# Optimization experiments

Hardware: AMD Instinct MI355X
Metric: run time of the kernel (lower is better)

The kernel has to match this reference:

```python
import jax, jax.numpy as jnp
import numpy as np

B, T, D, H = 4, 1024, 1024, 16
TP = 1024
HD = D // H
LN_EPS = 1e-3  # keras LayerNormalization default epsilon


def snac_linear(x, wt, mt):
    # conv1dsnac: w = tanh(wt) * sigmoid(mt), shape [1, nx, nf] -> [nx, nf]
    w = (jnp.tanh(wt) * jax.nn.sigmoid(mt))[0]
    return jnp.einsum('btx,xf->btf', x, w)


def layernorm(x, gamma, beta):
    mu = jnp.mean(x, axis=-1, keepdims=True)
    var = jnp.mean(jnp.square(x - mu), axis=-1, keepdims=True)
    return (x - mu) * jax.lax.rsqrt(var + LN_EPS) * gamma + beta


def setup_inputs() -> dict:
    key = jax.random.key(0)
    ks = jax.random.split(key, 10)
    s = 0.02
    return {
        'input': jax.random.normal(ks[0], (B, T, D), jnp.float32),
        'past': jax.random.normal(ks[1], (B, 2, H, TP, HD), jnp.float32),
        'qkv_wt': jax.random.normal(ks[2], (1, D, 3 * D), jnp.float32) * s,
        'qkv_mt': jax.random.normal(ks[3], (1, D, 3 * D), jnp.float32) * s,
        'merge_wt': jax.random.normal(ks[4], (1, D, D), jnp.float32) * s,
        'merge_mt': jax.random.normal(ks[5], (1, D, D), jnp.float32) * s,
        'ln1_wt': jax.random.normal(ks[6], (1, D, D), jnp.float32) * s,
        'ln1_mt': jax.random.normal(ks[7], (1, D, D), jnp.float32) * s,
        'g1': jnp.ones((D,), jnp.float32), 'b1': jnp.zeros((D,), jnp.float32),
        'g2': jnp.ones((D,), jnp.float32), 'b2': jnp.zeros((D,), jnp.float32),
    }


def reference(input, past, qkv_wt, qkv_mt, merge_wt, merge_mt, ln1_wt, ln1_mt, g1, b1, g2, b2):
    x = input
    xn = layernorm(x, g1, b1)
    c = snac_linear(xn, qkv_wt, qkv_mt)  # [B, T, 3D]
    q, k, v = jnp.split(c, 3, axis=2)
    # split heads -> [B, H, T, HD]
    to_heads = lambda t: t.reshape(B, T, H, HD).transpose(0, 2, 1, 3)
    q, k, v = to_heads(q), to_heads(k), to_heads(v)
    present = jnp.stack([k, v], axis=1)  # [B, 2, H, T, HD]
    pk, pv = past[:, 0], past[:, 1]
    k = jnp.concatenate([pk, k], axis=2)  # [B, H, TP+T, HD]
    v = jnp.concatenate([pv, v], axis=2)
    nd, ns = T, TP + T
    w = jnp.einsum('bhqd,bhkd->bhqk', q, k) * jax.lax.rsqrt(jnp.float32(HD))
    i = jnp.arange(nd)[:, None]
    j = jnp.arange(ns)[None, :]
    m = (i >= j - ns + nd).astype(w.dtype)  # [nd, ns] causal mask incl. past
    w = w * m - jnp.asarray(1e10, w.dtype) * (1 - m)
    msk = jax.nn.softmax(w, axis=-1)  # [B, H, T, TP+T]
    a = jnp.einsum('bhqk,bhkd->bhqd', msk, v)
    ah = a.transpose(0, 2, 1, 3).reshape(B, T, D)  # merge heads
    am = snac_linear(ah, merge_wt, merge_mt)
    xa = x + am
    mlp = snac_linear(layernorm(xa, g2, b2), ln1_wt, ln1_mt)
    xm = xa + mlp
    return xm, present, msk
```

## Files before the change

### kernel.cpp

```cpp
#include <hip/hip_runtime.h>
#include <hip/hip_bf16.h>

typedef _Float16 half8 __attribute__((ext_vector_type(8)));
typedef _Float16 half4v __attribute__((ext_vector_type(4)));
typedef float f32x4 __attribute__((ext_vector_type(4)));

#define DEV static __device__ __forceinline__


typedef __attribute__((address_space(1))) const unsigned int* gas_p;
typedef __attribute__((address_space(3))) unsigned int* las_p;
DEV void glds16(const void* g, void* s) {
  __builtin_amdgcn_global_load_lds((gas_p)g, (las_p)s, 16, 0, 0);
}

__global__ __launch_bounds__(256) void prep_all(const float* __restrict__ qkv_wt,
                                                const float* __restrict__ qkv_mt,
                                                const float* __restrict__ mg_wt,
                                                const float* __restrict__ mg_mt,
                                                const float* __restrict__ l1_wt,
                                                const float* __restrict__ l1_mt,
                                                _Float16* __restrict__ wq,
                                                _Float16* __restrict__ wm,
                                                _Float16* __restrict__ wl) {
  __shared__ float tile[64][65];
  const float *wt, *mt;
  _Float16* out;
  int N, bid;
  if (blockIdx.x < 768) {
    wt = qkv_wt; mt = qkv_mt; out = wq; N = 3072; bid = blockIdx.x;
  } else if (blockIdx.x < 1024) {
    wt = mg_wt; mt = mg_mt; out = wm; N = 1024; bid = blockIdx.x - 768;
  } else {
    wt = l1_wt; mt = l1_mt; out = wl; N = 1024; bid = blockIdx.x - 1024;
  }
  const int ntiles = N >> 6;
  const int nt = bid % ntiles, kt = bid / ntiles;
  const int k0 = kt << 6, n0 = nt << 6;
  const int t = threadIdx.x, r = t >> 2, c0 = (t & 3) << 4;
  const long ibase = (long)(k0 + r) * N + n0 + c0;
#pragma unroll
  for (int j = 0; j < 16; j += 4) {
    float4 a = *(const float4*)(wt + ibase + j);
    float4 b = *(const float4*)(mt + ibase + j);
    tile[r][c0 + j + 0] = tanhf(a.x) / (1.f + __expf(-b.x));
    tile[r][c0 + j + 1] = tanhf(a.y) / (1.f + __expf(-b.y));
    tile[r][c0 + j + 2] = tanhf(a.z) / (1.f + __expf(-b.z));
    tile[r][c0 + j + 3] = tanhf(a.w) / (1.f + __expf(-b.w));
  }
  __syncthreads();
  half8 o0, o1;
#pragma unroll
  for (int j = 0; j < 8; ++j) {
    o0[j] = (_Float16)tile[c0 + j][r];
    o1[j] = (_Float16)tile[c0 + 8 + j][r];
  }
  _Float16* dst = out + (long)(n0 + r) * 1024 + k0 + c0;
  *(half8*)dst = o0;
  *(half8*)(dst + 8) = o1;
}

__global__ __launch_bounds__(256) void kv_prep(const float* __restrict__ past,
                                               const _Float16* __restrict__ vnew,
                                               _Float16* __restrict__ kf,
                                               _Float16* __restrict__ vt) {
  __shared__ float tile[64][65];
  if (blockIdx.x < 4096) {
    const long e = ((long)blockIdx.x * 256 + threadIdx.x) * 4;
    const int b = (int)(e >> 20);
    const int rem = (int)(e & 1048575);
    float4 v = *(const float4*)(past + (long)b * 2097152 + rem);
    half4v o = {(_Float16)v.x, (_Float16)v.y, (_Float16)v.z, (_Float16)v.w};
    const int h = rem >> 16, td = rem & 65535;
    *(half4v*)(kf + (long)(b * 16 + h) * 131072 + td) = o;
    return;
  }
  const int bid = blockIdx.x - 4096;
  const int bh = bid >> 5, kt = bid & 31;
  const int b = bh >> 4, h = bh & 15;
  const int k0 = kt << 6;
  const int t = threadIdx.x, r = t >> 2, c0 = (t & 3) << 4;
  if (k0 < 1024) {
    const float* src = past + (((long)(b * 2 + 1) * 16 + h) * 1024 + (k0 + r)) * 64 + c0;
#pragma unroll
    for (int j = 0; j < 16; j += 4) {
      float4 v = *(const float4*)(src + j);
      tile[r][c0 + j + 0] = v.x;
      tile[r][c0 + j + 1] = v.y;
      tile[r][c0 + j + 2] = v.z;
      tile[r][c0 + j + 3] = v.w;
    }
  } else {
    const _Float16* src = vnew + ((long)bh * 1024 + (k0 - 1024 + r)) * 64 + c0;
    half8 a = *(const half8*)src;
    half8 bq = *(const half8*)(src + 8);
#pragma unroll
    for (int j = 0; j < 8; ++j) {
      tile[r][c0 + j] = (float)a[j];
      tile[r][c0 + 8 + j] = (float)bq[j];
    }
  }
  __syncthreads();
  half8 o0, o1;
#pragma unroll
  for (int j = 0; j < 8; ++j) {
    o0[j] = (_Float16)tile[c0 + j][r];
    o1[j] = (_Float16)tile[c0 + 8 + j][r];
  }
  _Float16* dst = vt + ((long)bh * 64 + r) * 2048 + k0 + c0;
  *(half8*)dst = o0;
  *(half8*)(dst + 8) = o1;
}

template <int F16IN>
__global__ __launch_bounds__(256) void ln_k(const void* __restrict__ xin,
                                            const float* __restrict__ g,
                                            const float* __restrict__ be,
                                            _Float16* __restrict__ out) {
  __shared__ float red[4];
  const int row = blockIdx.x, tid = threadIdx.x, l = tid & 63, w = tid >> 6;
  float v0, v1, v2, v3;
  if constexpr (F16IN == 0) {
    float4 v = *(const float4*)((const float*)xin + (long)row * 1024 + tid * 4);
    v0 = v.x; v1 = v.y; v2 = v.z; v3 = v.w;
  } else {
    half4v v = *(const half4v*)((const _Float16*)xin + (long)row * 1024 + tid * 4);
    v0 = (float)v[0]; v1 = (float)v[1]; v2 = (float)v[2]; v3 = (float)v[3];
  }
  float s = v0 + v1 + v2 + v3;
#pragma unroll
  for (int o = 32; o > 0; o >>= 1) s += __shfl_down(s, o, 64);
  if (l == 0) red[w] = s;
  __syncthreads();
  const float mu = (red[0] + red[1] + red[2] + red[3]) * (1.f / 1024.f);
  float dx = v0 - mu, dy = v1 - mu, dz = v2 - mu, dw = v3 - mu;
  float ss = dx * dx + dy * dy + dz * dz + dw * dw;
#pragma unroll
  for (int o = 32; o > 0; o >>= 1) ss += __shfl_down(ss, o, 64);
  __syncthreads();
  if (l == 0) red[w] = ss;
  __syncthreads();
  const float var = (red[0] + red[1] + red[2] + red[3]) * (1.f / 1024.f);
  const float rs = rsqrtf(var + 1e-3f);
  float4 gv = *(const float4*)(g + tid * 4);
  float4 bv = *(const float4*)(be + tid * 4);
  half4v o = {(_Float16)(dx * rs * gv.x + bv.x), (_Float16)(dy * rs * gv.y + bv.y),
              (_Float16)(dz * rs * gv.z + bv.z), (_Float16)(dw * rs * gv.w + bv.w)};
  *(half4v*)(out + (long)row * 1024 + tid * 4) = o;
}

template <int BM, int BN, int EPI>
__global__ __launch_bounds__(256) void gemm_k(const _Float16* __restrict__ A,
                                              const _Float16* __restrict__ Bt,
                                              int mtiles,
                                              _Float16* __restrict__ e_q,
                                              _Float16* __restrict__ e_k,
                                              _Float16* __restrict__ e_v,
                                              float* __restrict__ e_present,
                                              const void* __restrict__ e_resv,
                                              void* __restrict__ e_outv) {
  constexpr int FM = BM / 32, FN = BN / 32;
  __shared__ __align__(16) char smem[BM * 128 + BN * 128];
  char* As = smem;
  char* Bs = smem + BM * 128;
  const int tid = threadIdx.x, l = tid & 63, w = tid >> 6;
  const int wm = w >> 1, wn = w & 1;
  const int bm = blockIdx.x % mtiles, bn = blockIdx.x / mtiles;
  const long m0 = (long)bm * BM, n0 = (long)bn * BN;

  f32x4 acc[FM][FN];
#pragma unroll
  for (int i = 0; i < FM; ++i)
#pragma unroll
    for (int j = 0; j < FN; ++j) acc[i][j] = (f32x4){0.f, 0.f, 0.f, 0.f};

  for (int kt = 0; kt < 16; ++kt) {
#pragma unroll
    for (int i = 0; i < FM; ++i) {
      const int cid = i * 256 + tid, row = cid >> 3, u = cid & 7;
      glds16(A + (m0 + row) * 1024 + kt * 64 + ((u ^ (row & 7)) << 3),
             As + i * 4096 + w * 1024);
    }
#pragma unroll
    for (int i = 0; i < FN; ++i) {
      const int cid = i * 256 + tid, row = cid >> 3, u = cid & 7;
      glds16(Bt + (n0 + row) * 1024 + kt * 64 + ((u ^ (row & 7)) << 3),
             Bs + i * 4096 + w * 1024);
    }
    __syncthreads();
    __builtin_amdgcn_s_setprio(1);
#pragma unroll
    for (int k2 = 0; k2 < 2; ++k2) {
      const int sl = k2 * 4 + (l >> 4);
      half8 bfr[FN];
#pragma unroll
      for (int fn = 0; fn < FN; ++fn) {
        const int rn = wn * (BN / 2) + fn * 16 + (l & 15);
        bfr[fn] = *(const half8*)(Bs + rn * 128 + ((sl ^ (rn & 7)) << 4));
      }
#pragma unroll
      for (int fm = 0; fm < FM; ++fm) {
        const int rm = wm * (BM / 2) + fm * 16 + (l & 15);
        const half8 afr = *(const half8*)(As + rm * 128 + ((sl ^ (rm & 7)) << 4));
#pragma unroll
        for (int fn = 0; fn < FN; ++fn)
          acc[fm][fn] = __builtin_amdgcn_mfma_f32_16x16x32_f16(afr, bfr[fn], acc[fm][fn], 0, 0, 0);
      }
    }
    __builtin_amdgcn_s_setprio(0);
    __syncthreads();
  }
#pragma unroll
  for (int fm = 0; fm < FM; ++fm) {
#pragma unroll
    for (int fn = 0; fn < FN; ++fn) {
#pragma unroll
      for (int r = 0; r < 4; ++r) {
        const long row = m0 + wm * (BM / 2) + fm * 16 + (l >> 4) * 4 + r;
        const long col = n0 + wn * (BN / 2) + fn * 16 + (l & 15);
        const float v = acc[fm][fn][r];
        if constexpr (EPI == 0) {
          const int b = (int)(row >> 10), t = (int)(row & 1023);
          const int sec = (int)(col >> 10), h = ((int)col >> 6) & 15, hd = (int)col & 63;
          const long bh = b * 16 + h;
          if (sec == 0) {
            e_q[(bh * 1024 + t) * 64 + hd] = (_Float16)v;
          } else if (sec == 1) {
            e_present[(((long)(b * 2) * 16 + h) * 1024 + t) * 64 + hd] = v;
            e_k[(bh * 2048 + 1024 + t) * 64 + hd] = (_Float16)v;
          } else {
            e_present[(((long)(b * 2 + 1) * 16 + h) * 1024 + t) * 64 + hd] = v;
            e_v[(bh * 1024 + t) * 64 + hd] = (_Float16)v;
          }
        } else if constexpr (EPI == 1) {
          ((_Float16*)e_outv)[row * 1024 + col] =
              (_Float16)(((const float*)e_resv)[row * 1024 + col] + v);
        } else {
          ((float*)e_outv)[row * 1024 + col] =
              (float)((const _Float16*)e_resv)[row * 1024 + col] + v;
        }
      }
    }
  }
}

__global__ __launch_bounds__(256, 4) void attn_k(const _Float16* __restrict__ qg,
                                                 const _Float16* __restrict__ kg,
                                                 const _Float16* __restrict__ vtg,
                                                 float* __restrict__ msk,
                                                 _Float16* __restrict__ ah) {
  __shared__ __align__(16) char smem[40960];
  char* ps_all = smem + 32768;
  const int tid = threadIdx.x, l = tid & 63, w = tid >> 6;
  char* psw = ps_all + w * 2048;
  const int lq = l & 15, hi = l >> 4;

  const int x = blockIdx.x & 7, g = blockIdx.x >> 3;
  const int bh = (g & 7) * 8 + x;
  const int qt = 15 - (g >> 3);
  const int r0 = qt << 6;
  const int rowg0 = r0 + w * 16;

  const _Float16* kb = kg + (long)bh * 131072;
  const _Float16* vb = vtg + (long)bh * 131072;
  float* mskb = msk + ((long)bh * 1024 + rowg0) * 2048;

  half8 qa[2];
  {
    const _Float16* qp = qg + ((long)bh * 1024 + rowg0 + lq) * 64 + hi * 8;
    qa[0] = *(const half8*)qp;
    qa[1] = *(const half8*)(qp + 32);
  }

  constexpr float C1 = 0.125f * 1.44269504088896341f;
  const int lim = rowg0 + lq + 1024;

  const int nc1 = (r0 + 1215) >> 7;
  auto stageK128 = [&](int b, int c) {
#pragma unroll
    for (int i = 0; i < 4; ++i) {
      const int cid = i * 256 + tid, row = cid >> 3, u = cid & 7;
      glds16(kb + (long)(c * 128 + row) * 64 + ((u ^ (row & 7)) << 3),
             smem + b * 16384 + i * 4096 + w * 1024);
    }
  };
  float rsum = 0.f;
  stageK128(0, 0);
  __syncthreads();
  for (int c = 0; c < nc1; ++c) {
    const int cur = c & 1;
    if (c + 1 < nc1) stageK128(cur ^ 1, c + 1);
    const char* ks = smem + cur * 16384;
    f32x4 sa[8];
#pragma unroll
    for (int fn = 0; fn < 8; ++fn) sa[fn] = (f32x4){0.f, 0.f, 0.f, 0.f};
    __builtin_amdgcn_s_setprio(1);
#pragma unroll
    for (int k2 = 0; k2 < 2; ++k2) {
      const int sl = k2 * 4 + hi;
      half8 ak[8];
#pragma unroll
      for (int fn = 0; fn < 8; ++fn) {
        const int rn = fn * 16 + lq;
        ak[fn] = *(const half8*)(ks + rn * 128 + ((sl ^ (rn & 7)) << 4));
      }
#pragma unroll
      for (int fn = 0; fn < 8; ++fn)
        sa[fn] = __builtin_amdgcn_mfma_f32_16x16x32_f16(ak[fn], qa[k2], sa[fn], 0, 0, 0);
    }
    __builtin_amdgcn_s_setprio(0);
    if (c < nc1 - 1) {
#pragma unroll
      for (int fn = 0; fn < 8; ++fn)
#pragma unroll
        for (int r = 0; r < 4; ++r) rsum += __builtin_amdgcn_exp2f(sa[fn][r] * C1);
    } else {
#pragma unroll
      for (int fn = 0; fn < 8; ++fn)
#pragma unroll
        for (int r = 0; r < 4; ++r) {
          const int col = c * 128 + fn * 16 + hi * 4 + r;
          const float e = __builtin_amdgcn_exp2f(sa[fn][r] * C1);
          rsum += (col <= lim) ? e : 0.f;
        }
    }
    __syncthreads();
  }
  rsum += __shfl_xor(rsum, 16, 64);
  rsum += __shfl_xor(rsum, 32, 64);
  const float c2s = -__builtin_amdgcn_logf(rsum);

  const int nc = (r0 + 1151) >> 6;
  auto stageK = [&](int b, int c) {
#pragma unroll
    for (int i = 0; i < 2; ++i) {
      const int cid = i * 256 + tid, row = cid >> 3, u = cid & 7;
      glds16(kb + (long)(c * 64 + row) * 64 + ((u ^ (row & 7)) << 3),
             smem + b * 8192 + i * 4096 + w * 1024);
    }
  };
  auto stageV = [&](int b, int c) {
#pragma unroll
    for (int i = 0; i < 2; ++i) {
      const int cid = i * 256 + tid, row = cid >> 3, u = cid & 7;
      glds16(vb + (long)row * 2048 + c * 64 + ((u ^ (row & 7)) << 3),
             smem + 16384 + b * 8192 + i * 4096 + w * 1024);
    }
  };

  f32x4 pv[4];
#pragma unroll
  for (int j = 0; j < 4; ++j) pv[j] = (f32x4){0.f, 0.f, 0.f, 0.f};
  __syncthreads();
  stageK(0, 0);
  stageV(0, 0);
  __syncthreads();
  for (int c = 0; c < nc; ++c) {
    const int cur = c & 1;
    if (c + 1 < nc) {
      stageK(cur ^ 1, c + 1);
      stageV(cur ^ 1, c + 1);
    }
    const char* ks = smem + cur * 8192;
    f32x4 sa[4];
#pragma unroll
    for (int fn = 0; fn < 4; ++fn) sa[fn] = (f32x4){0.f, 0.f, 0.f, 0.f};
    __builtin_amdgcn_s_setprio(1);
#pragma unroll
    for (int k2 = 0; k2 < 2; ++k2) {
      const int sl = k2 * 4 + hi;
      half8 ak[4];
#pragma unroll
      for (int fn = 0; fn < 4; ++fn) {
        const int rn = fn * 16 + lq;
        ak[fn] = *(const half8*)(ks + rn * 128 + ((sl ^ (rn & 7)) << 4));
      }
#pragma unroll
      for (int fn = 0; fn < 4; ++fn)
        sa[fn] = __builtin_amdgcn_mfma_f32_16x16x32_f16(ak[fn], qa[k2], sa[fn], 0, 0, 0);
    }
    __builtin_amdgcn_s_setprio(0);
    const bool bound = (c == nc - 1);
#pragma unroll
    for (int fn = 0; fn < 4; ++fn) {
      float pr[4];
#pragma unroll
      for (int r = 0; r < 4; ++r) {
        float p = __builtin_amdgcn_exp2f(sa[fn][r] * C1 + c2s);
        if (bound) {
          const int col = c * 64 + fn * 16 + hi * 4 + r;
          p = (col <= lim) ? p : 0.f;
        }
        pr[r] = p;
      }
      *(float4*)(mskb + (long)lq * 2048 + c * 64 + fn * 16 + hi * 4) =
          make_float4(pr[0], pr[1], pr[2], pr[3]);
      const half4v hv = {(_Float16)pr[0], (_Float16)pr[1], (_Float16)pr[2],
                         (_Float16)pr[3]};
      const int bc = fn * 32 + hi * 8;
      *(half4v*)(psw + lq * 128 + ((((bc >> 4) ^ (lq & 7)) << 4) | (bc & 15))) = hv;
    }
    __builtin_amdgcn_wave_barrier();
    asm volatile("s_waitcnt lgkmcnt(0)" ::: "memory");
    __builtin_amdgcn_sched_barrier(0);
    const char* vs = smem + 16384 + cur * 8192;
    __builtin_amdgcn_s_setprio(1);
#pragma unroll
    for (int k2p = 0; k2p < 2; ++k2p) {
      const int sl2 = k2p * 4 + hi;
      const half8 pa = *(const half8*)(psw + lq * 128 + ((sl2 ^ (lq & 7)) << 4));
      half8 bv[4];
#pragma unroll
      for (int fn2 = 0; fn2 < 4; ++fn2) {
        const int rd = fn2 * 16 + lq;
        bv[fn2] = *(const half8*)(vs + rd * 128 + ((sl2 ^ (rd & 7)) << 4));
      }
#pragma unroll
      for (int fn2 = 0; fn2 < 4; ++fn2)
        pv[fn2] = __builtin_amdgcn_mfma_f32_16x16x32_f16(pa, bv[fn2], pv[fn2], 0, 0, 0);
    }
    __builtin_amdgcn_s_setprio(0);
    __syncthreads();
  }

  const int ntail = 512 - (nc << 4);
  if (ntail > 0) {
    const float4 z4 = make_float4(0.f, 0.f, 0.f, 0.f);
    for (int row = 0; row < 16; ++row)
      for (int i = l; i < ntail; i += 64)
        *(float4*)(mskb + (long)row * 2048 + nc * 64 + i * 4) = z4;
  }

  const int b_ = bh >> 4, h_ = bh & 15;
  _Float16* ahb = ah + ((long)b_ * 1024 + rowg0) * 1024 + h_ * 64;
#pragma unroll
  for (int fn2 = 0; fn2 < 4; ++fn2)
#pragma unroll
    for (int r = 0; r < 4; ++r)
      ahb[(long)(hi * 4 + r) * 1024 + fn2 * 16 + lq] = (_Float16)pv[fn2][r];
}

extern "C" void kernel_launch(void* const* d_in, const int* in_sizes, int n_in,
                              void* d_out, int out_size, void* d_ws, size_t ws_size,
                              hipStream_t stream) {
  const float* x = (const float*)d_in[0];
  const float* past = (const float*)d_in[1];
  const float* qkv_wt = (const float*)d_in[2];
  const float* qkv_mt = (const float*)d_in[3];
  const float* merge_wt = (const float*)d_in[4];
  const float* merge_mt = (const float*)d_in[5];
  const float* ln1_wt = (const float*)d_in[6];
  const float* ln1_mt = (const float*)d_in[7];
  const float* g1 = (const float*)d_in[8];
  const float* b1 = (const float*)d_in[9];
  const float* g2 = (const float*)d_in[10];
  const float* b2 = (const float*)d_in[11];

  float* out = (float*)d_out;
  float* o_xm = out;
  float* o_present = out + 4194304;
  float* o_msk = out + 4194304 + 8388608;

  char* ws = (char*)d_ws;
  _Float16* wq_t = (_Float16*)(ws + 0);
  _Float16* wm_t = (_Float16*)(ws + 6291456);
  _Float16* wl_t = (_Float16*)(ws + 8388608);
  _Float16* xn   = (_Float16*)(ws + 10485760);
  _Float16* qws  = (_Float16*)(ws + 18874368);
  _Float16* kful = (_Float16*)(ws + 27262976);
  _Float16* vnew = (_Float16*)(ws + 44040192);
  _Float16* vt   = (_Float16*)(ws + 52428800);
  _Float16* ah   = (_Float16*)(ws + 69206016);
  _Float16* xa   = (_Float16*)(ws + 77594624);

  prep_all<<<1280, 256, 0, stream>>>(qkv_wt, qkv_mt, merge_wt, merge_mt, ln1_wt,
                                     ln1_mt, wq_t, wm_t, wl_t);
  ln_k<0><<<4096, 256, 0, stream>>>(x, g1, b1, xn);
  gemm_k<128, 128, 0><<<768, 256, 0, stream>>>(xn, wq_t, 32, qws, kful, vnew,
                                               o_present, nullptr, nullptr);
  kv_prep<<<6144, 256, 0, stream>>>(past, vnew, kful, vt);
  attn_k<<<1024, 256, 0, stream>>>(qws, kful, vt, o_msk, ah);
  gemm_k<64, 64, 1><<<1024, 256, 0, stream>>>(ah, wm_t, 64, nullptr, nullptr,
                                              nullptr, nullptr, x, xa);
  ln_k<1><<<4096, 256, 0, stream>>>(xa, g2, b2, xn);
  gemm_k<64, 64, 2><<<1024, 256, 0, stream>>>(xn, wl_t, 64, nullptr, nullptr,
                                              nullptr, nullptr, xa, o_xm);
}
```

Measured before the change: 315.6 us.

## Double-buffer GEMM loads, fuse LN into weight prep, stream mask stores

The GEMM kernel now keeps two shared-memory stages, so the async global-to-LDS loads for the next K tile are issued while MFMAs run on the current one. The first LayerNorm is folded into the weight-prep kernel as extra blocks, which removes one launch. The large softmax-mask output is written with nontemporal stores to reduce cache pollution. The merge and MLP GEMMs switch to 64x128 tiles with half the blocks. The costs are doubled LDS use per block and fewer blocks for the smaller GEMMs, which may lower occupancy. The double-buffering also depends on correct waits and barriers at the end of each loop iteration.

```diff
diff --git a/kernel.cpp b/kernel.cpp
--- a/kernel.cpp
+++ b/kernel.cpp
@@ -13,17 +13,50 @@
 DEV void glds16(const void* g, void* s) {
   __builtin_amdgcn_global_load_lds((gas_p)g, (las_p)s, 16, 0, 0);
 }
-
-__global__ __launch_bounds__(256) void prep_all(const float* __restrict__ qkv_wt,
-                                                const float* __restrict__ qkv_mt,
-                                                const float* __restrict__ mg_wt,
-                                                const float* __restrict__ mg_mt,
-                                                const float* __restrict__ l1_wt,
-                                                const float* __restrict__ l1_mt,
-                                                _Float16* __restrict__ wq,
-                                                _Float16* __restrict__ wm,
-                                                _Float16* __restrict__ wl) {
+DEV void nt_store4(float* p, f32x4 v) {
+  __builtin_nontemporal_store(v, (f32x4*)p);
+}
+
+__global__ __launch_bounds__(256) void prep_ln(const float* __restrict__ qkv_wt,
+                                               const float* __restrict__ qkv_mt,
+                                               const float* __restrict__ mg_wt,
+                                               const float* __restrict__ mg_mt,
+                                               const float* __restrict__ l1_wt,
+                                               const float* __restrict__ l1_mt,
+                                               _Float16* __restrict__ wq,
+                                               _Float16* __restrict__ wm,
+                                               _Float16* __restrict__ wl,
+                                               const float* __restrict__ x,
+                                               const float* __restrict__ g1,
+                                               const float* __restrict__ b1,
+                                               _Float16* __restrict__ xn) {
   __shared__ float tile[64][65];
+  if (blockIdx.x >= 1280) {
+    float* red = &tile[0][0];
+    const int row = blockIdx.x - 1280, tid = threadIdx.x, l = tid & 63, w = tid >> 6;
+    float4 v = *(const float4*)(x + (long)row * 1024 + tid * 4);
+    float s = v.x + v.y + v.z + v.w;
+#pragma unroll
+    for (int o = 32; o > 0; o >>= 1) s += __shfl_down(s, o, 64);
+    if (l == 0) red[w] = s;
+    __syncthreads();
+    const float mu = (red[0] + red[1] + red[2] + red[3]) * (1.f / 1024.f);
+    float dx = v.x - mu, dy = v.y - mu, dz = v.z - mu, dw = v.w - mu;
+    float ss = dx * dx + dy * dy + dz * dz + dw * dw;
+#pragma unroll
+    for (int o = 32; o > 0; o >>= 1) ss += __shfl_down(ss, o, 64);
+    __syncthreads();
+    if (l == 0) red[w] = ss;
+    __syncthreads();
+    const float var = (red[0] + red[1] + red[2] + red[3]) * (1.f / 1024.f);
+    const float rs = rsqrtf(var + 1e-3f);
+    float4 gv = *(const float4*)(g1 + tid * 4);
+    float4 bv = *(const float4*)(b1 + tid * 4);
+    half4v o = {(_Float16)(dx * rs * gv.x + bv.x), (_Float16)(dy * rs * gv.y + bv.y),
+                (_Float16)(dz * rs * gv.z + bv.z), (_Float16)(dw * rs * gv.w + bv.w)};
+    *(half4v*)(xn + (long)row * 1024 + tid * 4) = o;
+    return;
+  }
   const float *wt, *mt;
   _Float16* out;
   int N, bid;
@@ -112,21 +145,14 @@
   *(half8*)(dst + 8) = o1;
 }
 
-template <int F16IN>
-__global__ __launch_bounds__(256) void ln_k(const void* __restrict__ xin,
+__global__ __launch_bounds__(256) void ln_k(const _Float16* __restrict__ xin,
                                             const float* __restrict__ g,
                                             const float* __restrict__ be,
                                             _Float16* __restrict__ out) {
   __shared__ float red[4];
   const int row = blockIdx.x, tid = threadIdx.x, l = tid & 63, w = tid >> 6;
-  float v0, v1, v2, v3;
-  if constexpr (F16IN == 0) {
-    float4 v = *(const float4*)((const float*)xin + (long)row * 1024 + tid * 4);
-    v0 = v.x; v1 = v.y; v2 = v.z; v3 = v.w;
-  } else {
-    half4v v = *(const half4v*)((const _Float16*)xin + (long)row * 1024 + tid * 4);
-    v0 = (float)v[0]; v1 = (float)v[1]; v2 = (float)v[2]; v3 = (float)v[3];
-  }
+  half4v v = *(const half4v*)(xin + (long)row * 1024 + tid * 4);
+  float v0 = (float)v[0], v1 = (float)v[1], v2 = (float)v[2], v3 = (float)v[3];
   float s = v0 + v1 + v2 + v3;
 #pragma unroll
   for (int o = 32; o > 0; o >>= 1) s += __shfl_down(s, o, 64);
@@ -160,9 +186,8 @@
                                               const void* __restrict__ e_resv,
                                               void* __restrict__ e_outv) {
   constexpr int FM = BM / 32, FN = BN / 32;
-  __shared__ __align__(16) char smem[BM * 128 + BN * 128];
-  char* As = smem;
-  char* Bs = smem + BM * 128;
+  __shared__ __align__(16) char smem[2 * BM * 128 + 2 * BN * 128];
+  char* Bbase = smem + 2 * BM * 128;
   const int tid = threadIdx.x, l = tid & 63, w = tid >> 6;
   const int wm = w >> 1, wn = w & 1;
   const int bm = blockIdx.x % mtiles, bn = blockIdx.x / mtiles;
@@ -174,20 +199,28 @@
 #pragma unroll
     for (int j = 0; j < FN; ++j) acc[i][j] = (f32x4){0.f, 0.f, 0.f, 0.f};
 
-  for (int kt = 0; kt < 16; ++kt) {
+  auto stage = [&](int b, int kt) {
 #pragma unroll
     for (int i = 0; i < FM; ++i) {
       const int cid = i * 256 + tid, row = cid >> 3, u = cid & 7;
       glds16(A + (m0 + row) * 1024 + kt * 64 + ((u ^ (row & 7)) << 3),
-             As + i * 4096 + w * 1024);
+             smem + b * BM * 128 + i * 4096 + w * 1024);
     }
 #pragma unroll
     for (int i = 0; i < FN; ++i) {
       const int cid = i * 256 + tid, row = cid >> 3, u = cid & 7;
       glds16(Bt + (n0 + row) * 1024 + kt * 64 + ((u ^ (row & 7)) << 3),
-             Bs + i * 4096 + w * 1024);
-    }
-    __syncthreads();
+             Bbase + b * BN * 128 + i * 4096 + w * 1024);
+    }
+  };
+
+  stage(0, 0);
+  __syncthreads();
+  for (int kt = 0; kt < 16; ++kt) {
+    const int cur = kt & 1;
+    if (kt < 15) stage(cur ^ 1, kt + 1);
+    const char* As = smem + cur * BM * 128;
+    const char* Bs = Bbase + cur * BN * 128;
     __builtin_amdgcn_s_setprio(1);
 #pragma unroll
     for (int k2 = 0; k2 < 2; ++k2) {
@@ -393,8 +426,8 @@
         }
         pr[r] = p;
       }
-      *(float4*)(mskb + (long)lq * 2048 + c * 64 + fn * 16 + hi * 4) =
-          make_float4(pr[0], pr[1], pr[2], pr[3]);
+      nt_store4(mskb + (long)lq * 2048 + c * 64 + fn * 16 + hi * 4,
+                (f32x4){pr[0], pr[1], pr[2], pr[3]});
       const half4v hv = {(_Float16)pr[0], (_Float16)pr[1], (_Float16)pr[2],
                          (_Float16)pr[3]};
       const int bc = fn * 32 + hi * 8;
@@ -425,10 +458,10 @@
 
   const int ntail = 512 - (nc << 4);
   if (ntail > 0) {
-    const float4 z4 = make_float4(0.f, 0.f, 0.f, 0.f);
     for (int row = 0; row < 16; ++row)
       for (int i = l; i < ntail; i += 64)
-        *(float4*)(mskb + (long)row * 2048 + nc * 64 + i * 4) = z4;
+        nt_store4(mskb + (long)row * 2048 + nc * 64 + i * 4,
+                  (f32x4){0.f, 0.f, 0.f, 0.f});
   }
 
   const int b_ = bh >> 4, h_ = bh & 15;
@@ -473,16 +506,15 @@
   _Float16* ah   = (_Float16*)(ws + 69206016);
   _Float16* xa   = (_Float16*)(ws + 77594624);
 
-  prep_all<<<1280, 256, 0, stream>>>(qkv_wt, qkv_mt, merge_wt, merge_mt, ln1_wt,
-                                     ln1_mt, wq_t, wm_t, wl_t);
-  ln_k<0><<<4096, 256, 0, stream>>>(x, g1, b1, xn);
+  prep_ln<<<5376, 256, 0, stream>>>(qkv_wt, qkv_mt, merge_wt, merge_mt, ln1_wt,
+                                    ln1_mt, wq_t, wm_t, wl_t, x, g1, b1, xn);
   gemm_k<128, 128, 0><<<768, 256, 0, stream>>>(xn, wq_t, 32, qws, kful, vnew,
                                                o_present, nullptr, nullptr);
   kv_prep<<<6144, 256, 0, stream>>>(past, vnew, kful, vt);
   attn_k<<<1024, 256, 0, stream>>>(qws, kful, vt, o_msk, ah);
-  gemm_k<64, 64, 1><<<1024, 256, 0, stream>>>(ah, wm_t, 64, nullptr, nullptr,
+  gemm_k<64, 128, 1><<<512, 256, 0, stream>>>(ah, wm_t, 64, nullptr, nullptr,
                                               nullptr, nullptr, x, xa);
-  ln_k<1><<<4096, 256, 0, stream>>>(xa, g2, b2, xn);
-  gemm_k<64, 64, 2><<<1024, 256, 0, stream>>>(xn, wl_t, 64, nullptr, nullptr,
+  ln_k<<<4096, 256, 0, stream>>>(xa, g2, b2, xn);
+  gemm_k<64, 128, 2><<<512, 256, 0, stream>>>(xn, wl_t, 64, nullptr, nullptr,
                                               nullptr, nullptr, xa, o_xm);
 }
```

Result: faster. 306.6 us (-2.8%).

## Double-buffer GEMM LDS, hoist past KV conversion into prep kernel, widen N tiles

Applied to the files above, without the earlier changes.

The GEMM kernel now double-buffers its LDS tiles, issuing async global-to-LDS loads for the next k-tile while computing the current one. The past-only K and V conversion is moved into the weight-prep kernel so it no longer waits behind the QKV GEMM. Only the new V transpose stays in a small late kernel. The merge and MLP GEMMs use 64x128 tiles with half as many blocks. Doubling LDS use may lower occupancy, and the larger tiles reduce the block count to 512.

```diff
diff --git a/kernel.cpp b/kernel.cpp
--- a/kernel.cpp
+++ b/kernel.cpp
@@ -22,8 +22,48 @@
                                                 const float* __restrict__ l1_mt,
                                                 _Float16* __restrict__ wq,
                                                 _Float16* __restrict__ wm,
-                                                _Float16* __restrict__ wl) {
+                                                _Float16* __restrict__ wl,
+                                                const float* __restrict__ past,
+                                                _Float16* __restrict__ kf,
+                                                _Float16* __restrict__ vt) {
   __shared__ float tile[64][65];
+  if (blockIdx.x >= 1280 && blockIdx.x < 5376) {
+    const long e = ((long)(blockIdx.x - 1280) * 256 + threadIdx.x) * 4;
+    const int b = (int)(e >> 20);
+    const int rem = (int)(e & 1048575);
+    float4 v = *(const float4*)(past + (long)b * 2097152 + rem);
+    half4v o = {(_Float16)v.x, (_Float16)v.y, (_Float16)v.z, (_Float16)v.w};
+    const int h = rem >> 16, td = rem & 65535;
+    *(half4v*)(kf + (long)(b * 16 + h) * 131072 + td) = o;
+    return;
+  }
+  if (blockIdx.x >= 5376) {
+    const int bid = blockIdx.x - 5376;
+    const int bh = bid >> 4, kt = bid & 15;
+    const int b = bh >> 4, h = bh & 15;
+    const int k0 = kt << 6;
+    const int t = threadIdx.x, r = t >> 2, c0 = (t & 3) << 4;
+    const float* src = past + (((long)(b * 2 + 1) * 16 + h) * 1024 + (k0 + r)) * 64 + c0;
+#pragma unroll
+    for (int j = 0; j < 16; j += 4) {
+      float4 v = *(const float4*)(src + j);
+      tile[r][c0 + j + 0] = v.x;
+      tile[r][c0 + j + 1] = v.y;
+      tile[r][c0 + j + 2] = v.z;
+      tile[r][c0 + j + 3] = v.w;
+    }
+    __syncthreads();
+    half8 o0, o1;
+#pragma unroll
+    for (int j = 0; j < 8; ++j) {
+      o0[j] = (_Float16)tile[c0 + j][r];
+      o1[j] = (_Float16)tile[c0 + 8 + j][r];
+    }
+    _Float16* dst = vt + ((long)bh * 64 + r) * 2048 + k0 + c0;
+    *(half8*)dst = o0;
+    *(half8*)(dst + 8) = o1;
+    return;
+  }
   const float *wt, *mt;
   _Float16* out;
   int N, bid;
@@ -60,45 +100,20 @@
   *(half8*)(dst + 8) = o1;
 }
 
-__global__ __launch_bounds__(256) void kv_prep(const float* __restrict__ past,
-                                               const _Float16* __restrict__ vnew,
-                                               _Float16* __restrict__ kf,
+__global__ __launch_bounds__(256) void kv_late(const _Float16* __restrict__ vnew,
                                                _Float16* __restrict__ vt) {
   __shared__ float tile[64][65];
-  if (blockIdx.x < 4096) {
-    const long e = ((long)blockIdx.x * 256 + threadIdx.x) * 4;
-    const int b = (int)(e >> 20);
-    const int rem = (int)(e & 1048575);
-    float4 v = *(const float4*)(past + (long)b * 2097152 + rem);
-    half4v o = {(_Float16)v.x, (_Float16)v.y, (_Float16)v.z, (_Float16)v.w};
-    const int h = rem >> 16, td = rem & 65535;
-    *(half4v*)(kf + (long)(b * 16 + h) * 131072 + td) = o;
-    return;
-  }
-  const int bid = blockIdx.x - 4096;
-  const int bh = bid >> 5, kt = bid & 31;
-  const int b = bh >> 4, h = bh & 15;
+  const int bid = blockIdx.x;
+  const int bh = bid >> 4, kt = 16 + (bid & 15);
   const int k0 = kt << 6;
   const int t = threadIdx.x, r = t >> 2, c0 = (t & 3) << 4;
-  if (k0 < 1024) {
-    const float* src = past + (((long)(b * 2 + 1) * 16 + h) * 1024 + (k0 + r)) * 64 + c0;
-#pragma unroll
-    for (int j = 0; j < 16; j += 4) {
-      float4 v = *(const float4*)(src + j);
-      tile[r][c0 + j + 0] = v.x;
-      tile[r][c0 + j + 1] = v.y;
-      tile[r][c0 + j + 2] = v.z;
-      tile[r][c0 + j + 3] = v.w;
-    }
-  } else {
-    const _Float16* src = vnew + ((long)bh * 1024 + (k0 - 1024 + r)) * 64 + c0;
-    half8 a = *(const half8*)src;
-    half8 bq = *(const half8*)(src + 8);
-#pragma unroll
-    for (int j = 0; j < 8; ++j) {
-      tile[r][c0 + j] = (float)a[j];
-      tile[r][c0 + 8 + j] = (float)bq[j];
-    }
+  const _Float16* src = vnew + ((long)bh * 1024 + (k0 - 1024 + r)) * 64 + c0;
+  half8 a = *(const half8*)src;
+  half8 bq = *(const half8*)(src + 8);
+#pragma unroll
+  for (int j = 0; j < 8; ++j) {
+    tile[r][c0 + j] = (float)a[j];
+    tile[r][c0 + 8 + j] = (float)bq[j];
   }
   __syncthreads();
   half8 o0, o1;
@@ -160,9 +175,8 @@
                                               const void* __restrict__ e_resv,
                                               void* __restrict__ e_outv) {
   constexpr int FM = BM / 32, FN = BN / 32;
-  __shared__ __align__(16) char smem[BM * 128 + BN * 128];
-  char* As = smem;
-  char* Bs = smem + BM * 128;
+  __shared__ __align__(16) char smem[2 * BM * 128 + 2 * BN * 128];
+  char* Bbase = smem + 2 * BM * 128;
   const int tid = threadIdx.x, l = tid & 63, w = tid >> 6;
   const int wm = w >> 1, wn = w & 1;
   const int bm = blockIdx.x % mtiles, bn = blockIdx.x / mtiles;
@@ -174,20 +188,28 @@
 #pragma unroll
     for (int j = 0; j < FN; ++j) acc[i][j] = (f32x4){0.f, 0.f, 0.f, 0.f};
 
-  for (int kt = 0; kt < 16; ++kt) {
+  auto stage = [&](int b, int kt) {
 #pragma unroll
     for (int i = 0; i < FM; ++i) {
       const int cid = i * 256 + tid, row = cid >> 3, u = cid & 7;
       glds16(A + (m0 + row) * 1024 + kt * 64 + ((u ^ (row & 7)) << 3),
-             As + i * 4096 + w * 1024);
+             smem + b * BM * 128 + i * 4096 + w * 1024);
     }
 #pragma unroll
     for (int i = 0; i < FN; ++i) {
       const int cid = i * 256 + tid, row = cid >> 3, u = cid & 7;
       glds16(Bt + (n0 + row) * 1024 + kt * 64 + ((u ^ (row & 7)) << 3),
-             Bs + i * 4096 + w * 1024);
-    }
-    __syncthreads();
+             Bbase + b * BN * 128 + i * 4096 + w * 1024);
+    }
+  };
+
+  stage(0, 0);
+  __syncthreads();
+  for (int kt = 0; kt < 16; ++kt) {
+    const int cur = kt & 1;
+    if (kt < 15) stage(cur ^ 1, kt + 1);
+    const char* As = smem + cur * BM * 128;
+    const char* Bs = Bbase + cur * BN * 128;
     __builtin_amdgcn_s_setprio(1);
 #pragma unroll
     for (int k2 = 0; k2 < 2; ++k2) {
@@ -473,16 +495,16 @@
   _Float16* ah   = (_Float16*)(ws + 69206016);
   _Float16* xa   = (_Float16*)(ws + 77594624);
 
-  prep_all<<<1280, 256, 0, stream>>>(qkv_wt, qkv_mt, merge_wt, merge_mt, ln1_wt,
-                                     ln1_mt, wq_t, wm_t, wl_t);
+  prep_all<<<6400, 256, 0, stream>>>(qkv_wt, qkv_mt, merge_wt, merge_mt, ln1_wt,
+                                     ln1_mt, wq_t, wm_t, wl_t, past, kful, vt);
   ln_k<0><<<4096, 256, 0, stream>>>(x, g1, b1, xn);
   gemm_k<128, 128, 0><<<768, 256, 0, stream>>>(xn, wq_t, 32, qws, kful, vnew,
                                                o_present, nullptr, nullptr);
-  kv_prep<<<6144, 256, 0, stream>>>(past, vnew, kful, vt);
+  kv_late<<<1024, 256, 0, stream>>>(vnew, vt);
   attn_k<<<1024, 256, 0, stream>>>(qws, kful, vt, o_msk, ah);
-  gemm_k<64, 64, 1><<<1024, 256, 0, stream>>>(ah, wm_t, 64, nullptr, nullptr,
+  gemm_k<64, 128, 1><<<512, 256, 0, stream>>>(ah, wm_t, 64, nullptr, nullptr,
                                               nullptr, nullptr, x, xa);
   ln_k<1><<<4096, 256, 0, stream>>>(xa, g2, b2, xn);
-  gemm_k<64, 64, 2><<<1024, 256, 0, stream>>>(xn, wl_t, 64, nullptr, nullptr,
+  gemm_k<64, 128, 2><<<512, 256, 0, stream>>>(xn, wl_t, 64, nullptr, nullptr,
                                               nullptr, nullptr, xa, o_xm);
 }
```

New measurement: 289.5 us. -8.3%, faster.
